# Performance work log

Hardware: AMD Instinct MI355X
Metric: run time of the kernel (lower is better)

## Reference

```python
import jax, jax.numpy as jnp
import numpy as np

RATE = 1.2           # midpoint of rate_range (original draws uniformly per call)
N_FREQ = 1025
HOP = 1024           # hop_length kwarg (default n_fft//2 = (n_freq-1))
TWO_PI = 2.0 * np.pi


def setup_inputs() -> dict:
    key = jax.random.key(0)
    k1, k2 = jax.random.split(key)
    shape = (16, N_FREQ, 2048)
    return {
        "spec_real": jax.random.normal(k1, shape, dtype=jnp.float32),
        "spec_imag": jax.random.normal(k2, shape, dtype=jnp.float32),
    }


def reference(spec_real, spec_imag):
    # phase vocoder (torchaudio.functional.phase_vocoder) with fixed rate,
    # followed by abs() since return_complex=False.
    T = spec_real.shape[-1]
    phase_advance = jnp.linspace(0.0, np.pi * HOP, N_FREQ, dtype=spec_real.dtype)[:, None]  # [F,1]

    # static because RATE is a Python float -> jit-safe output shape
    time_steps = jnp.arange(0, T, RATE, dtype=spec_real.dtype)  # [T_out]
    alphas = time_steps % 1.0                                    # [T_out]
    idx = time_steps.astype(jnp.int32)                           # floor indices

    # phase of the very first frame
    phase_0 = jnp.arctan2(spec_imag[..., :1], spec_real[..., :1])  # [B,F,1]

    # pad time dim by 2 (as torchaudio does), then gather the two neighbors
    pad = [(0, 0)] * (spec_real.ndim - 1) + [(0, 2)]
    re = jnp.pad(spec_real, pad)
    im = jnp.pad(spec_imag, pad)
    re0, im0 = re[..., idx], im[..., idx]          # [B,F,T_out]
    re1, im1 = re[..., idx + 1], im[..., idx + 1]

    angle_0 = jnp.arctan2(im0, re0)
    angle_1 = jnp.arctan2(im1, re1)
    norm_0 = jnp.sqrt(re0 * re0 + im0 * im0)
    norm_1 = jnp.sqrt(re1 * re1 + im1 * im1)

    # phase difference, unwrapped to (-pi, pi], plus expected advance
    phase = angle_1 - angle_0 - phase_advance
    phase = phase - TWO_PI * jnp.round(phase / TWO_PI)
    phase = phase + phase_advance

    # accumulate phase starting from phase_0
    phase = jnp.concatenate([phase_0, phase[..., :-1]], axis=-1)
    phase_acc = jnp.cumsum(phase, axis=-1)

    # linear magnitude interpolation
    mag = alphas * norm_1 + (1.0 - alphas) * norm_0

    out_re = mag * jnp.cos(phase_acc)
    out_im = mag * jnp.sin(phase_acc)
    # return_complex=False -> torch.abs of the complex reconstruction
    return jnp.sqrt(out_re * out_re + out_im * out_im)
```

## Files before the change

### kernel.cpp

```cpp
#include <hip/hip_runtime.h>


#define T_IN   2048
#define T_OUT  1707
#define UPT    10
#define IPT    12
#define UPR    171

typedef float vf4 __attribute__((ext_vector_type(4)));
typedef float vf2 __attribute__((ext_vector_type(2)));

__global__ __launch_bounds__(192) void pv_wave_kernel(
    const float* __restrict__ re, const float* __restrict__ im,
    float* __restrict__ out) {
    __shared__ __align__(16) float lds[3][640];

    const int row  = blockIdx.x;
    const int tid  = threadIdx.x;
    const int wv   = tid >> 6;
    const int lane = tid & 63;
    const int vr   = (wv << 6) + lane;

    if (vr < UPR) {
        const float* __restrict__ rr = re + (size_t)row * T_IN + IPT * vr;
        const float* __restrict__ ir = im + (size_t)row * T_IN + IPT * vr;

        float r[IPT], q[IPT];
        if (vr < UPR - 1) {
            float4 a0 = ((const float4*)rr)[0];
            float4 a1 = ((const float4*)rr)[1];
            float4 a2 = ((const float4*)rr)[2];
            float4 b0 = ((const float4*)ir)[0];
            float4 b1 = ((const float4*)ir)[1];
            float4 b2 = ((const float4*)ir)[2];
            r[0]=a0.x; r[1]=a0.y; r[2]=a0.z;  r[3]=a0.w;
            r[4]=a1.x; r[5]=a1.y; r[6]=a1.z;  r[7]=a1.w;
            r[8]=a2.x; r[9]=a2.y; r[10]=a2.z; r[11]=a2.w;
            q[0]=b0.x; q[1]=b0.y; q[2]=b0.z;  q[3]=b0.w;
            q[4]=b1.x; q[5]=b1.y; q[6]=b1.z;  q[7]=b1.w;
            q[8]=b2.x; q[9]=b2.y; q[10]=b2.z; q[11]=b2.w;
        } else {
            float4 a0 = ((const float4*)rr)[0];
            float4 a1 = ((const float4*)rr)[1];
            float4 b0 = ((const float4*)ir)[0];
            float4 b1 = ((const float4*)ir)[1];
            r[0]=a0.x; r[1]=a0.y; r[2]=a0.z; r[3]=a0.w;
            r[4]=a1.x; r[5]=a1.y; r[6]=a1.z; r[7]=a1.w;
            r[8]=0.0f; r[9]=0.0f; r[10]=0.0f; r[11]=0.0f;
            q[0]=b0.x; q[1]=b0.y; q[2]=b0.z; q[3]=b0.w;
            q[4]=b1.x; q[5]=b1.y; q[6]=b1.z; q[7]=b1.w;
            q[8]=0.0f; q[9]=0.0f; q[10]=0.0f; q[11]=0.0f;
        }

        float n[IPT];
#pragma unroll
        for (int k = 0; k < IPT; ++k) n[k] = sqrtf(r[k] * r[k] + q[k] * q[k]);

        const int L[UPT] = {0, 1, 2, 3, 4, 6, 7, 8, 9, 10};
        const float tb = (float)(IPT * vr);
        float o[UPT];
#pragma unroll
        for (int s = 0; s < UPT; ++s) {
            float tf = (float)(UPT * vr + s) * 1.2f;
            float a  = tf - (tb + (float)L[s]);
            o[s] = a * n[L[s] + 1] + (1.0f - a) * n[L[s]];
        }

        float* slice = lds[wv];
#pragma unroll
        for (int s2 = 0; s2 < 5; ++s2) {
            vf2 v; v.x = o[2 * s2]; v.y = o[2 * s2 + 1];
            *(vf2*)&slice[UPT * lane + 2 * s2] = v;
        }
    }

    const int u0  = wv << 6;
    const int cnt = (u0 + 64 < UPR) ? 640 : (T_OUT - UPT * u0);
    float* __restrict__ gbase = out + (size_t)row * T_OUT + (size_t)(UPT * u0);
    const float* slice = lds[wv];
#pragma unroll
    for (int p = 0; p < 3; ++p) {
        int off = (p << 8) + (lane << 2);
        if (off + 4 <= cnt) {
            vf4 v = *(const vf4*)&slice[off];
            __builtin_nontemporal_store(v, (vf4*)(gbase + off));
        } else if (off < cnt) {
            for (int t = off; t < cnt; ++t)
                __builtin_nontemporal_store(slice[t], gbase + t);
        }
    }
}

extern "C" void kernel_launch(void* const* d_in, const int* in_sizes, int n_in,
                              void* d_out, int out_size, void* d_ws, size_t ws_size,
                              hipStream_t stream) {
    const float* re = (const float*)d_in[0];
    const float* im = (const float*)d_in[1];
    float* out = (float*)d_out;

    const int nrows = in_sizes[0] / T_IN;
    pv_wave_kernel<<<nrows, 192, 0, stream>>>(re, im, out);
}
```

Before: 61.96 us.

## Load input with dense coalesced float4 groups and redistribute norms via lane shuffles

Replaces per-thread strided 48-byte loads with a layout where each group of four lanes reads contiguous float4 chunks, so a wavefront covers a dense address range. The magnitudes are computed on the loaded chunks and then exchanged between the four lanes with xor shuffles so each thread ends up with its original 12 contiguous norms. The aim is fuller use of each memory transaction, at the cost of extra shuffle and select instructions.

```diff
diff --git a/kernel.cpp b/kernel.cpp
--- a/kernel.cpp
+++ b/kernel.cpp
@@ -10,7 +10,7 @@
 typedef float vf4 __attribute__((ext_vector_type(4)));
 typedef float vf2 __attribute__((ext_vector_type(2)));
 
-__global__ __launch_bounds__(192) void pv_wave_kernel(
+__global__ __launch_bounds__(192) void pv_dense_kernel(
     const float* __restrict__ re, const float* __restrict__ im,
     float* __restrict__ out) {
     __shared__ __align__(16) float lds[3][640];
@@ -19,43 +19,52 @@
     const int tid  = threadIdx.x;
     const int wv   = tid >> 6;
     const int lane = tid & 63;
-    const int vr   = (wv << 6) + lane;
+    const int G    = tid >> 2;
+    const int j    = tid & 3;
 
+    const float* __restrict__ rbase = re + (size_t)row * T_IN;
+    const float* __restrict__ ibase = im + (size_t)row * T_IN;
+
+    float4 ra[3], ia[3];
+#pragma unroll
+    for (int p = 0; p < 3; ++p) {
+        int f = 48 * G + 4 * j + 16 * p;
+        if (f < T_IN) {
+            ra[p] = *(const float4*)(rbase + f);
+            ia[p] = *(const float4*)(ibase + f);
+        } else {
+            ra[p] = make_float4(0.f, 0.f, 0.f, 0.f);
+            ia[p] = make_float4(0.f, 0.f, 0.f, 0.f);
+        }
+    }
+
+    float n0[4], n1[4], n2[4];
+    {
+        const float* r0 = &ra[0].x; const float* q0 = &ia[0].x;
+        const float* r1 = &ra[1].x; const float* q1 = &ia[1].x;
+        const float* r2 = &ra[2].x; const float* q2 = &ia[2].x;
+#pragma unroll
+        for (int k = 0; k < 4; ++k) {
+            n0[k] = sqrtf(r0[k] * r0[k] + q0[k] * q0[k]);
+            n1[k] = sqrtf(r1[k] * r1[k] + q1[k] * q1[k]);
+            n2[k] = sqrtf(r2[k] * r2[k] + q2[k] * q2[k]);
+        }
+    }
+
+    float n[IPT];
+#pragma unroll
+    for (int k = 0; k < 4; ++k) {
+        float s1 = (j == 0) ? n1[k] : (j == 1) ? n0[k] : (j == 2) ? n2[k] : n1[k];
+        float B  = __shfl_xor(s1, 1);
+        float s2 = (j < 2) ? n2[k] : n0[k];
+        float r2 = __shfl_xor(s2, 2);
+        float A  = (j & 1) ? r2 : ((j == 0) ? n0[k] : n1[k]);
+        float C  = (j & 1) ? ((j == 1) ? n1[k] : n2[k]) : r2;
+        n[k] = A; n[4 + k] = B; n[8 + k] = C;
+    }
+
+    const int vr = tid;
     if (vr < UPR) {
-        const float* __restrict__ rr = re + (size_t)row * T_IN + IPT * vr;
-        const float* __restrict__ ir = im + (size_t)row * T_IN + IPT * vr;
-
-        float r[IPT], q[IPT];
-        if (vr < UPR - 1) {
-            float4 a0 = ((const float4*)rr)[0];
-            float4 a1 = ((const float4*)rr)[1];
-            float4 a2 = ((const float4*)rr)[2];
-            float4 b0 = ((const float4*)ir)[0];
-            float4 b1 = ((const float4*)ir)[1];
-            float4 b2 = ((const float4*)ir)[2];
-            r[0]=a0.x; r[1]=a0.y; r[2]=a0.z;  r[3]=a0.w;
-            r[4]=a1.x; r[5]=a1.y; r[6]=a1.z;  r[7]=a1.w;
-            r[8]=a2.x; r[9]=a2.y; r[10]=a2.z; r[11]=a2.w;
-            q[0]=b0.x; q[1]=b0.y; q[2]=b0.z;  q[3]=b0.w;
-            q[4]=b1.x; q[5]=b1.y; q[6]=b1.z;  q[7]=b1.w;
-            q[8]=b2.x; q[9]=b2.y; q[10]=b2.z; q[11]=b2.w;
-        } else {
-            float4 a0 = ((const float4*)rr)[0];
-            float4 a1 = ((const float4*)rr)[1];
-            float4 b0 = ((const float4*)ir)[0];
-            float4 b1 = ((const float4*)ir)[1];
-            r[0]=a0.x; r[1]=a0.y; r[2]=a0.z; r[3]=a0.w;
-            r[4]=a1.x; r[5]=a1.y; r[6]=a1.z; r[7]=a1.w;
-            r[8]=0.0f; r[9]=0.0f; r[10]=0.0f; r[11]=0.0f;
-            q[0]=b0.x; q[1]=b0.y; q[2]=b0.z; q[3]=b0.w;
-            q[4]=b1.x; q[5]=b1.y; q[6]=b1.z; q[7]=b1.w;
-            q[8]=0.0f; q[9]=0.0f; q[10]=0.0f; q[11]=0.0f;
-        }
-
-        float n[IPT];
-#pragma unroll
-        for (int k = 0; k < IPT; ++k) n[k] = sqrtf(r[k] * r[k] + q[k] * q[k]);
-
         const int L[UPT] = {0, 1, 2, 3, 4, 6, 7, 8, 9, 10};
         const float tb = (float)(IPT * vr);
         float o[UPT];
@@ -65,7 +74,6 @@
             float a  = tf - (tb + (float)L[s]);
             o[s] = a * n[L[s] + 1] + (1.0f - a) * n[L[s]];
         }
-
         float* slice = lds[wv];
 #pragma unroll
         for (int s2 = 0; s2 < 5; ++s2) {
@@ -99,5 +107,5 @@
     float* out = (float*)d_out;
 
     const int nrows = in_sizes[0] / T_IN;
-    pv_wave_kernel<<<nrows, 192, 0, stream>>>(re, im, out);
+    pv_dense_kernel<<<nrows, 192, 0, stream>>>(re, im, out);
 }
```

Result: slower. 66.85 us (+7.9%).

## Stage magnitudes in LDS with fully coalesced float4 row loads

Applied to the files above, without the earlier changes.

Each block of 256 threads now loads the whole input row with contiguous float4 reads, computes magnitudes, and stores them to shared memory. After a barrier, the interpolating threads read their 12 magnitudes from LDS instead of issuing strided 48-byte global loads. This aims to improve load coalescing and spread the sqrt work across more threads. The cost is an extra barrier and LDS round trip, plus a fourth wave that is idle in the interpolation and store phases.

```diff
diff --git a/kernel.cpp b/kernel.cpp
--- a/kernel.cpp
+++ b/kernel.cpp
@@ -10,83 +10,82 @@
 typedef float vf4 __attribute__((ext_vector_type(4)));
 typedef float vf2 __attribute__((ext_vector_type(2)));
 
-__global__ __launch_bounds__(192) void pv_wave_kernel(
+__global__ __launch_bounds__(256) void pv_lds_kernel(
     const float* __restrict__ re, const float* __restrict__ im,
     float* __restrict__ out) {
-    __shared__ __align__(16) float lds[3][640];
+    __shared__ __align__(16) float n[T_IN + 16];
+    __shared__ __align__(16) float ob[3][640];
 
     const int row  = blockIdx.x;
     const int tid  = threadIdx.x;
     const int wv   = tid >> 6;
     const int lane = tid & 63;
-    const int vr   = (wv << 6) + lane;
 
-    if (vr < UPR) {
-        const float* __restrict__ rr = re + (size_t)row * T_IN + IPT * vr;
-        const float* __restrict__ ir = im + (size_t)row * T_IN + IPT * vr;
+    const float4* __restrict__ re4 = (const float4*)(re + (size_t)row * T_IN);
+    const float4* __restrict__ im4 = (const float4*)(im + (size_t)row * T_IN);
 
-        float r[IPT], q[IPT];
-        if (vr < UPR - 1) {
-            float4 a0 = ((const float4*)rr)[0];
-            float4 a1 = ((const float4*)rr)[1];
-            float4 a2 = ((const float4*)rr)[2];
-            float4 b0 = ((const float4*)ir)[0];
-            float4 b1 = ((const float4*)ir)[1];
-            float4 b2 = ((const float4*)ir)[2];
-            r[0]=a0.x; r[1]=a0.y; r[2]=a0.z;  r[3]=a0.w;
-            r[4]=a1.x; r[5]=a1.y; r[6]=a1.z;  r[7]=a1.w;
-            r[8]=a2.x; r[9]=a2.y; r[10]=a2.z; r[11]=a2.w;
-            q[0]=b0.x; q[1]=b0.y; q[2]=b0.z;  q[3]=b0.w;
-            q[4]=b1.x; q[5]=b1.y; q[6]=b1.z;  q[7]=b1.w;
-            q[8]=b2.x; q[9]=b2.y; q[10]=b2.z; q[11]=b2.w;
-        } else {
-            float4 a0 = ((const float4*)rr)[0];
-            float4 a1 = ((const float4*)rr)[1];
-            float4 b0 = ((const float4*)ir)[0];
-            float4 b1 = ((const float4*)ir)[1];
-            r[0]=a0.x; r[1]=a0.y; r[2]=a0.z; r[3]=a0.w;
-            r[4]=a1.x; r[5]=a1.y; r[6]=a1.z; r[7]=a1.w;
-            r[8]=0.0f; r[9]=0.0f; r[10]=0.0f; r[11]=0.0f;
-            q[0]=b0.x; q[1]=b0.y; q[2]=b0.z; q[3]=b0.w;
-            q[4]=b1.x; q[5]=b1.y; q[6]=b1.z; q[7]=b1.w;
-            q[8]=0.0f; q[9]=0.0f; q[10]=0.0f; q[11]=0.0f;
-        }
+#pragma unroll
+    for (int k = 0; k < 2; ++k) {
+        int v = (k << 8) + tid;
+        float4 r = re4[v];
+        float4 q = im4[v];
+        vf4 m;
+        m.x = sqrtf(r.x * r.x + q.x * q.x);
+        m.y = sqrtf(r.y * r.y + q.y * q.y);
+        m.z = sqrtf(r.z * r.z + q.z * q.z);
+        m.w = sqrtf(r.w * r.w + q.w * q.w);
+        *(vf4*)&n[v << 2] = m;
+    }
+    if (tid < 4) {
+        vf4 z = {0.f, 0.f, 0.f, 0.f};
+        *(vf4*)&n[T_IN + (tid << 2)] = z;
+    }
+    __syncthreads();
 
-        float n[IPT];
-#pragma unroll
-        for (int k = 0; k < IPT; ++k) n[k] = sqrtf(r[k] * r[k] + q[k] * q[k]);
+    if (tid < UPR) {
+        const int u = tid;
+        vf4 na = *(const vf4*)&n[IPT * u];
+        vf4 nb = *(const vf4*)&n[IPT * u + 4];
+        vf4 nc = *(const vf4*)&n[IPT * u + 8];
+        float nn[IPT];
+        nn[0]=na.x; nn[1]=na.y; nn[2] =na.z; nn[3] =na.w;
+        nn[4]=nb.x; nn[5]=nb.y; nn[6] =nb.z; nn[7] =nb.w;
+        nn[8]=nc.x; nn[9]=nc.y; nn[10]=nc.z; nn[11]=nc.w;
 
         const int L[UPT] = {0, 1, 2, 3, 4, 6, 7, 8, 9, 10};
-        const float tb = (float)(IPT * vr);
+        const float tb = (float)(IPT * u);
         float o[UPT];
 #pragma unroll
         for (int s = 0; s < UPT; ++s) {
-            float tf = (float)(UPT * vr + s) * 1.2f;
+            float tf = (float)(UPT * u + s) * 1.2f;
             float a  = tf - (tb + (float)L[s]);
-            o[s] = a * n[L[s] + 1] + (1.0f - a) * n[L[s]];
+            o[s] = a * nn[L[s] + 1] + (1.0f - a) * nn[L[s]];
         }
-
-        float* slice = lds[wv];
+        float* slice = ob[wv];
 #pragma unroll
         for (int s2 = 0; s2 < 5; ++s2) {
-            vf2 v; v.x = o[2 * s2]; v.y = o[2 * s2 + 1];
-            *(vf2*)&slice[UPT * lane + 2 * s2] = v;
+            vf2 v2; v2.x = o[2 * s2]; v2.y = o[2 * s2 + 1];
+            *(vf2*)&slice[UPT * lane + 2 * s2] = v2;
         }
     }
 
-    const int u0  = wv << 6;
-    const int cnt = (u0 + 64 < UPR) ? 640 : (T_OUT - UPT * u0);
-    float* __restrict__ gbase = out + (size_t)row * T_OUT + (size_t)(UPT * u0);
-    const float* slice = lds[wv];
+    asm volatile("s_waitcnt lgkmcnt(0)" ::: "memory");
+
+    if (wv < 3) {
+        const int u0  = wv << 6;
+        const int cnt = (wv < 2) ? 640 : (T_OUT - UPT * u0);
+        float* __restrict__ gbase = out + (size_t)row * T_OUT + (size_t)(UPT * u0);
+        const float* slice = ob[wv];
 #pragma unroll
-    for (int p = 0; p < 3; ++p) {
-        int off = (p << 8) + (lane << 2);
-        if (off + 4 <= cnt) {
-            vf4 v = *(const vf4*)&slice[off];
-            __builtin_nontemporal_store(v, (vf4*)(gbase + off));
-        } else if (off < cnt) {
-            for (int t = off; t < cnt; ++t)
-                __builtin_nontemporal_store(slice[t], gbase + t);
+        for (int p = 0; p < 3; ++p) {
+            int off = (p << 8) + (lane << 2);
+            if (off + 4 <= cnt) {
+                vf4 v = *(const vf4*)&slice[off];
+                __builtin_nontemporal_store(v, (vf4*)(gbase + off));
+            } else if (off < cnt) {
+                for (int t = off; t < cnt; ++t)
+                    __builtin_nontemporal_store(slice[t], gbase + t);
+            }
         }
     }
 }
@@ -99,5 +98,5 @@
     float* out = (float*)d_out;
 
     const int nrows = in_sizes[0] / T_IN;
-    pv_wave_kernel<<<nrows, 192, 0, stream>>>(re, im, out);
+    pv_lds_kernel<<<nrows, 256, 0, stream>>>(re, im, out);
 }
```

Measured after the change: 60.66 us. 2.1% less time.
